# Optimization experiments

Hardware: AMD Instinct MI355X
Metric: run time of the kernel (lower is better)

## Reference

```python
import jax, jax.numpy as jnp
import numpy as np

N, IN, HID, OUT = 8192, 512, 256, 128

def setup_inputs() -> dict:
    key = jax.random.key(0)
    k1, k2, k3, k4 = jax.random.split(key, 4)
    adj = jax.random.uniform(k1, (N, N), dtype=jnp.float32)
    feature = jax.random.normal(k2, (N, IN), dtype=jnp.float32)
    W1 = jax.random.normal(k3, (IN, HID), dtype=jnp.float32) * (1.0 / np.sqrt(IN))
    b1 = jnp.zeros((HID,), dtype=jnp.float32)
    W2 = jax.random.normal(k4, (HID, OUT), dtype=jnp.float32) * (1.0 / np.sqrt(HID))
    b2 = jnp.zeros((OUT,), dtype=jnp.float32)
    return {"adj": adj, "feature": feature, "W1": W1, "b1": b1, "W2": W2, "b2": b2}

def reference(adj, feature, W1, b1, W2, b2):
    # GCN encoder: layer1 (relu) then layer2 (linear output)
    h = jax.nn.relu(adj @ (feature @ W1) + b1)   # [N, HID]
    h = adj @ (h @ W2) + b2                      # [N, OUT]
    # InnerProductDecoder: sigmoid(flatten(h @ h.T))
    logits = h @ h.T                             # [N, N]
    h_noise = jax.nn.sigmoid(logits.reshape(-1)) # [N*N]
    return (h_noise, h)
```

## Files before the change

kernel.cpp:

```cpp
#include <hip/hip_runtime.h>


typedef __bf16 bf16x8_t __attribute__((ext_vector_type(8)));
typedef __bf16 bf16x4_t __attribute__((ext_vector_type(4)));
typedef float  f32x4_t  __attribute__((ext_vector_type(4)));

#define MFMA_BF16(a, b, c) __builtin_amdgcn_mfma_f32_16x16x32_bf16((a), (b), (c), 0, 0, 0)

__device__ __forceinline__ bf16x8_t cvt8(f32x4_t u, f32x4_t v) {
    bf16x8_t o;
    o[0] = (__bf16)u[0]; o[1] = (__bf16)u[1]; o[2] = (__bf16)u[2]; o[3] = (__bf16)u[3];
    o[4] = (__bf16)v[0]; o[5] = (__bf16)v[1]; o[6] = (__bf16)v[2]; o[7] = (__bf16)v[3];
    return o;
}

__device__ __forceinline__ f32x4_t nt_load4(const float* p) {
    return __builtin_nontemporal_load((const f32x4_t*)p);
}
__device__ __forceinline__ void nt_store4(f32x4_t v, float* p) {
    __builtin_nontemporal_store(v, (f32x4_t*)p);
}

template<int AUX>
__device__ __forceinline__ void gload_lds16(const float* g, float* l) {
    __builtin_amdgcn_global_load_lds(
        (const __attribute__((address_space(1))) unsigned int*)g,
        (__attribute__((address_space(3))) unsigned int*)l, 16, 0, AUX);
}

__global__ __launch_bounds__(256) void cast_all(
    const float* __restrict__ feat, const float* __restrict__ W1,
    const float* __restrict__ W2, __bf16* __restrict__ fb,
    __bf16* __restrict__ w1t, __bf16* __restrict__ w2t)
{
    const int j = blockIdx.x * 256 + threadIdx.x;
    if (j < 524288) {
        const float* p = feat + (size_t)j * 8;
        f32x4_t u = nt_load4(p);
        f32x4_t v = nt_load4(p + 4);
        *(bf16x8_t*)(fb + (size_t)j * 8) = cvt8(u, v);
    } else if (j < 524288 + 131072) {
        int t = j - 524288;
        int k = t >> 8, n = t & 255;
        w1t[n * 512 + k] = (__bf16)W1[t];
    } else if (j < 524288 + 131072 + 32768) {
        int t = j - 655360;
        int k = t >> 7, n = t & 127;
        w2t[n * 256 + k] = (__bf16)W2[t];
    }
}

template<int MT, int WC>
__global__ __launch_bounds__(256, 2) void gemm_bt_cbf16(
    const __bf16* __restrict__ X, const __bf16* __restrict__ Yb,
    __bf16* __restrict__ C, int K, int N)
{
    constexpr int WR = 4 / WC;
    constexpr int BM = WR * MT * 16;
    constexpr int BN = WC * 64;
    const int mblk = blockIdx.x, nblk = blockIdx.y;
    const int w = threadIdx.x >> 6, lane = threadIdx.x & 63;
    const int wr = w / WC, wc = w % WC;
    const int q = lane >> 4, l16 = lane & 15;
    const int mbase = mblk * BM + wr * (MT * 16);
    const int nbase = nblk * BN + wc * 64;

    f32x4_t acc[MT][4];
    const f32x4_t z = {0.f, 0.f, 0.f, 0.f};
#pragma unroll
    for (int i = 0; i < MT; i++)
#pragma unroll
        for (int jj = 0; jj < 4; jj++) acc[i][jj] = z;

    const __bf16* Xr[MT];
    const __bf16* Yr[4];
#pragma unroll
    for (int i = 0; i < MT; i++) Xr[i] = X + (size_t)(mbase + i * 16 + l16) * K + q * 8;
#pragma unroll
    for (int jj = 0; jj < 4; jj++) Yr[jj] = Yb + (size_t)(nbase + jj * 16 + l16) * K + q * 8;

    for (int k = 0; k < K; k += 32) {
        bf16x8_t a[MT], b[4];
#pragma unroll
        for (int i = 0; i < MT; i++) a[i] = *(const bf16x8_t*)(Xr[i] + k);
#pragma unroll
        for (int jj = 0; jj < 4; jj++) b[jj] = *(const bf16x8_t*)(Yr[jj] + k);
#pragma unroll
        for (int i = 0; i < MT; i++)
#pragma unroll
            for (int jj = 0; jj < 4; jj++) acc[i][jj] = MFMA_BF16(a[i], b[jj], acc[i][jj]);
    }

#pragma unroll
    for (int i = 0; i < MT; i++)
#pragma unroll
        for (int jj = 0; jj < 4; jj++) {
            const int row0 = mbase + i * 16 + q * 4;
            const int col = nbase + jj * 16 + l16;
#pragma unroll
            for (int r = 0; r < 4; r++)
                C[(size_t)(row0 + r) * N + col] = (__bf16)acc[i][jj][r];
        }
}

template<int NN>
__global__ __launch_bounds__(256, 2) void gemm_adj_lds(
    const float* __restrict__ A, const __bf16* __restrict__ Y,
    float* __restrict__ P, int kchunk)
{
    constexpr int NT = NN / 64;
    __shared__ float As[2][4096];

    const int mblk = blockIdx.x;
    const int ks = blockIdx.y;
    const int w = threadIdx.x >> 6, lane = threadIdx.x & 63;
    const int q = lane >> 4, l16 = lane & 15;
    const int kbase = ks * kchunk;
    const int ntiles = kchunk >> 6;

    const int lrow = lane >> 4;
    const int lg = lane & 15;
    const float* gsrc[4];
    int loff[4];
#pragma unroll
    for (int j = 0; j < 4; j++) {
        const int row = j * 16 + w * 4 + lrow;
        const int colswz = ((lg ^ (row & 15)) << 2);
        gsrc[j] = A + (size_t)(mblk * 64 + row) * 8192 + kbase + colswz;
        loff[j] = row * 64 + (lg << 2);
    }

    const __bf16* Yr[NT];
#pragma unroll
    for (int jj = 0; jj < NT; jj++)
        Yr[jj] = Y + (size_t)(w * (NN / 4) + jj * 16 + l16) * 8192 + q * 8;

    f32x4_t acc[4][NT];
    const f32x4_t z = {0.f, 0.f, 0.f, 0.f};
#pragma unroll
    for (int i = 0; i < 4; i++)
#pragma unroll
        for (int jj = 0; jj < NT; jj++) acc[i][jj] = z;

#pragma unroll
    for (int j = 0; j < 4; j++) gload_lds16<2>(gsrc[j], &As[0][0] + loff[j]);

    int buf = 0;
    for (int kt = 0; kt < ntiles; kt++) {
        const int kk = kbase + (kt << 6);

        bf16x8_t breg[2][NT];
#pragma unroll
        for (int s = 0; s < 2; s++)
#pragma unroll
            for (int jj = 0; jj < NT; jj++)
                breg[s][jj] = *(const bf16x8_t*)(Yr[jj] + kk + s * 32);

        __syncthreads();

        if (kt + 1 < ntiles) {
            const int koff = (kt + 1) << 6;
#pragma unroll
            for (int j = 0; j < 4; j++)
                gload_lds16<2>(gsrc[j] + koff, &As[buf ^ 1][0] + loff[j]);
        }

        const float* __restrict__ L = &As[buf][0];
#pragma unroll
        for (int s = 0; s < 2; s++) {
            bf16x8_t a[4];
#pragma unroll
            for (int i = 0; i < 4; i++) {
                const int r = i * 16 + l16;
                const int g0 = ((s * 8 + q * 2) ^ l16) << 2;
                const int g1 = ((s * 8 + q * 2 + 1) ^ l16) << 2;
                f32x4_t u = *(const f32x4_t*)(L + r * 64 + g0);
                f32x4_t v = *(const f32x4_t*)(L + r * 64 + g1);
                a[i] = cvt8(u, v);
            }
#pragma unroll
            for (int i = 0; i < 4; i++)
#pragma unroll
                for (int jj = 0; jj < NT; jj++)
                    acc[i][jj] = MFMA_BF16(a[i], breg[s][jj], acc[i][jj]);
        }
        buf ^= 1;
    }

#pragma unroll
    for (int i = 0; i < 4; i++)
#pragma unroll
        for (int jj = 0; jj < NT; jj++) {
            const int row0 = mblk * 64 + i * 16 + q * 4;
            const int col = w * (NN / 4) + jj * 16 + l16;
            float* pp = P + ((size_t)ks * 8192 + row0) * NN + col;
#pragma unroll
            for (int r = 0; r < 4; r++)
                __builtin_nontemporal_store(acc[i][jj][r], pp + (size_t)r * NN);
        }
}

__global__ __launch_bounds__(256) void epi_relu_bias(
    const float* __restrict__ P, const float* __restrict__ bias,
    __bf16* __restrict__ H)
{
    const size_t SL = (size_t)8192 * 256;
    const size_t idx = ((size_t)blockIdx.x * 256 + threadIdx.x) * 4;
    f32x4_t s0 = nt_load4(P + idx);
    f32x4_t s1 = nt_load4(P + SL + idx);
    f32x4_t s2 = nt_load4(P + 2 * SL + idx);
    f32x4_t s3 = nt_load4(P + 3 * SL + idx);
    const int col = (int)(idx & 255);
    f32x4_t bb = *(const f32x4_t*)(bias + col);
    bf16x4_t o;
#pragma unroll
    for (int e = 0; e < 4; e++)
        o[e] = (__bf16)fmaxf(s0[e] + s1[e] + s2[e] + s3[e] + bb[e], 0.f);
    *(bf16x4_t*)(H + idx) = o;
}

__global__ __launch_bounds__(256) void epi_bias_out(
    const float* __restrict__ P, const float* __restrict__ bias,
    float* __restrict__ Hout, __bf16* __restrict__ Hbf)
{
    const size_t SL = (size_t)8192 * 128;
    const size_t idx = ((size_t)blockIdx.x * 256 + threadIdx.x) * 4;
    f32x4_t s0 = nt_load4(P + idx);
    f32x4_t s1 = nt_load4(P + SL + idx);
    f32x4_t s2 = nt_load4(P + 2 * SL + idx);
    f32x4_t s3 = nt_load4(P + 3 * SL + idx);
    const int col = (int)(idx & 127);
    f32x4_t bb = *(const f32x4_t*)(bias + col);
    f32x4_t o;
#pragma unroll
    for (int e = 0; e < 4; e++)
        o[e] = s0[e] + s1[e] + s2[e] + s3[e] + bb[e];
    nt_store4(o, Hout + idx);
    bf16x4_t ob;
#pragma unroll
    for (int e = 0; e < 4; e++) ob[e] = (__bf16)o[e];
    *(bf16x4_t*)(Hbf + idx) = ob;
}

__global__ __launch_bounds__(256, 2) void gemm_sig(
    const __bf16* __restrict__ H, float* __restrict__ out)
{
    const int mblk = blockIdx.x, nblk = blockIdx.y;
    const int w = threadIdx.x >> 6, lane = threadIdx.x & 63;
    const int wr = w >> 1, wc = w & 1;
    const int q = lane >> 4, l16 = lane & 15;
    const int mbase = mblk * 128 + wr * 64;
    const int nbase = nblk * 128 + wc * 64;

    f32x4_t acc[4][4];
    const f32x4_t z = {0.f, 0.f, 0.f, 0.f};
#pragma unroll
    for (int i = 0; i < 4; i++)
#pragma unroll
        for (int jj = 0; jj < 4; jj++) acc[i][jj] = z;

#pragma unroll
    for (int k = 0; k < 128; k += 32) {
        bf16x8_t a[4], b[4];
#pragma unroll
        for (int i = 0; i < 4; i++)
            a[i] = *(const bf16x8_t*)(H + (size_t)(mbase + i * 16 + l16) * 128 + k + q * 8);
#pragma unroll
        for (int jj = 0; jj < 4; jj++)
            b[jj] = *(const bf16x8_t*)(H + (size_t)(nbase + jj * 16 + l16) * 128 + k + q * 8);
#pragma unroll
        for (int i = 0; i < 4; i++)
#pragma unroll
            for (int jj = 0; jj < 4; jj++) acc[i][jj] = MFMA_BF16(a[i], b[jj], acc[i][jj]);
    }

#pragma unroll
    for (int i = 0; i < 4; i++)
#pragma unroll
        for (int jj = 0; jj < 4; jj++) {
            const int row0 = mbase + i * 16 + q * 4;
            const int col = nbase + jj * 16 + l16;
#pragma unroll
            for (int r = 0; r < 4; r++) {
                float x = acc[i][jj][r];
                float s = 1.0f / (1.0f + __expf(-x));
                __builtin_nontemporal_store(s, out + (size_t)(row0 + r) * 8192 + col);
            }
        }
}

extern "C" void kernel_launch(void* const* d_in, const int* in_sizes, int n_in,
                              void* d_out, int out_size, void* d_ws, size_t ws_size,
                              hipStream_t stream)
{
    const float* adj  = (const float*)d_in[0];
    const float* feat = (const float*)d_in[1];
    const float* W1   = (const float*)d_in[2];
    const float* b1   = (const float*)d_in[3];
    const float* W2   = (const float*)d_in[4];
    const float* b2   = (const float*)d_in[5];
    float* out = (float*)d_out;

    char* p = (char*)d_ws;
    __bf16* featbf = (__bf16*)p; p += (size_t)8192 * 512 * 2;
    __bf16* W1T    = (__bf16*)p; p += (size_t)256 * 512 * 2;
    __bf16* W2T    = (__bf16*)p; p += (size_t)128 * 256 * 2;
    __bf16* t1T    = (__bf16*)p; p += (size_t)256 * 8192 * 2;
    __bf16* h1     = (__bf16*)p; p += (size_t)8192 * 256 * 2;
    __bf16* t2T    = (__bf16*)p; p += (size_t)128 * 8192 * 2;
    __bf16* hbf    = (__bf16*)p; p += (size_t)8192 * 128 * 2;
    float* part    = (float*)p;

    cast_all<<<2688, 256, 0, stream>>>(feat, W1, W2, featbf, W1T, W2T);
    gemm_bt_cbf16<2, 2><<<dim3(4, 64), 256, 0, stream>>>(W1T, featbf, t1T, 512, 8192);
    gemm_adj_lds<256><<<dim3(128, 4), 256, 0, stream>>>(adj, t1T, part, 2048);
    epi_relu_bias<<<2048, 256, 0, stream>>>(part, b1, h1);
    gemm_bt_cbf16<2, 2><<<dim3(2, 64), 256, 0, stream>>>(W2T, h1, t2T, 256, 8192);
    gemm_adj_lds<128><<<dim3(128, 4), 256, 0, stream>>>(adj, t2T, part, 2048);
    epi_bias_out<<<1024, 256, 0, stream>>>(part, b2, out + (size_t)8192 * 8192, hbf);
    gemm_sig<<<dim3(64, 64), 256, 0, stream>>>(hbf, out);
}
```

Measured before the change: 636.7 us.

## Stage sigmoid output through LDS for vectorized coalesced stores, raise occupancy

The sigmoid-GEMM epilogue now writes its results into a padded shared-memory tile in two halves, then reads them back as 16-byte vectors and issues coalesced nontemporal float4 stores to the 256MB output, replacing scattered scalar stores. The launch-bounds occupancy hint rises from 2 to 4 blocks. The split-K partial-store loop in the first GEMM is reordered so consecutive stores go along a row. This targets write efficiency on the dominant output stream, at the cost of extra LDS traffic, barriers and register pressure.

```diff
diff --git a/kernel.cpp b/kernel.cpp
--- a/kernel.cpp
+++ b/kernel.cpp
@@ -188,16 +188,16 @@
     }
 
 #pragma unroll
-    for (int i = 0; i < 4; i++)
-#pragma unroll
-        for (int jj = 0; jj < NT; jj++) {
-            const int row0 = mblk * 64 + i * 16 + q * 4;
-            const int col = w * (NN / 4) + jj * 16 + l16;
-            float* pp = P + ((size_t)ks * 8192 + row0) * NN + col;
-#pragma unroll
-            for (int r = 0; r < 4; r++)
-                __builtin_nontemporal_store(acc[i][jj][r], pp + (size_t)r * NN);
-        }
+    for (int i = 0; i < 4; i++) {
+        const int row0 = mblk * 64 + i * 16 + q * 4;
+#pragma unroll
+        for (int r = 0; r < 4; r++) {
+            float* pp = P + ((size_t)ks * 8192 + row0 + r) * NN + w * (NN / 4) + l16;
+#pragma unroll
+            for (int jj = 0; jj < NT; jj++)
+                __builtin_nontemporal_store(acc[i][jj][r], pp + jj * 16);
+        }
+    }
 }
 
 __global__ __launch_bounds__(256) void epi_relu_bias(
@@ -242,9 +242,11 @@
     *(bf16x4_t*)(Hbf + idx) = ob;
 }
 
-__global__ __launch_bounds__(256, 2) void gemm_sig(
+__global__ __launch_bounds__(256, 4) void gemm_sig(
     const __bf16* __restrict__ H, float* __restrict__ out)
 {
+    __shared__ float S[64 * 132];
+
     const int mblk = blockIdx.x, nblk = blockIdx.y;
     const int w = threadIdx.x >> 6, lane = threadIdx.x & 63;
     const int wr = w >> 1, wc = w & 1;
@@ -275,18 +277,34 @@
     }
 
 #pragma unroll
-    for (int i = 0; i < 4; i++)
-#pragma unroll
-        for (int jj = 0; jj < 4; jj++) {
-            const int row0 = mbase + i * 16 + q * 4;
-            const int col = nbase + jj * 16 + l16;
-#pragma unroll
-            for (int r = 0; r < 4; r++) {
-                float x = acc[i][jj][r];
-                float s = 1.0f / (1.0f + __expf(-x));
-                __builtin_nontemporal_store(s, out + (size_t)(row0 + r) * 8192 + col);
+    for (int h = 0; h < 2; h++) {
+        if (h) __syncthreads();
+#pragma unroll
+        for (int i = 0; i < 2; i++) {
+            const int ii = h * 2 + i;
+            const int lrow = wr * 32 + i * 16 + q * 4;
+#pragma unroll
+            for (int jj = 0; jj < 4; jj++) {
+                const int col = wc * 64 + jj * 16 + l16;
+#pragma unroll
+                for (int r = 0; r < 4; r++) {
+                    const float x = acc[ii][jj][r];
+                    S[(lrow + r) * 132 + col] = 1.0f / (1.0f + __expf(-x));
+                }
             }
         }
+        __syncthreads();
+#pragma unroll
+        for (int it = 0; it < 8; it++) {
+            const int gid = it * 256 + (int)threadIdx.x;
+            const int lr = gid >> 5;
+            const int qd = gid & 31;
+            f32x4_t v = *(const f32x4_t*)(S + lr * 132 + qd * 4);
+            const int grow = mblk * 128 + (lr >> 5) * 64 + (lr & 31) + h * 32;
+            const int gcol = nblk * 128 + qd * 4;
+            nt_store4(v, out + (size_t)grow * 8192 + gcol);
+        }
+    }
 }
 
 extern "C" void kernel_launch(void* const* d_in, const int* in_sizes, int n_in,
```

After: 639.3 us. No clear change (+0.4%).
